# Kernel tuning notes

Measured on AMD Instinct MI355X. Metric: run time of the kernel, lower is better.

Reference implementation:

```python
import jax, jax.numpy as jnp
import numpy as np

NEG_SLOPE = 0.2
LN_EPS = 1e-6

B, L, D, H = 32, 512, 256, 4
N = B * L
E = 65536
C = D  # per-head out channels (GATConv out_channels=d_model)


def setup_inputs() -> dict:
    key = jax.random.key(0)
    ks = jax.random.split(key, 10)
    s = 1.0 / np.sqrt(D)
    inputs = jax.random.normal(ks[0], (B, L, D), dtype=jnp.float32)
    edge_index = jax.random.randint(ks[1], (2, E), 0, N, dtype=jnp.int64)
    return {
        "inputs": inputs,
        "edge_index": edge_index,
        "ln_gamma": jnp.ones((D,), jnp.float32),
        "ln_beta": jnp.zeros((D,), jnp.float32),
        "W1": jax.random.normal(ks[2], (D, D), jnp.float32) * s,   # linear_before_gnn
        "b1": jnp.zeros((D,), jnp.float32),
        "W_gat": jax.random.normal(ks[3], (H * C, D), jnp.float32) * s,  # GATConv.lin (no bias)
        "att_src": jax.random.normal(ks[4], (H, C), jnp.float32) * s,
        "att_dst": jax.random.normal(ks[5], (H, C), jnp.float32) * s,
        "bias_gat": jnp.zeros((C,), jnp.float32),  # concat=False -> size out_channels
        "W2": jax.random.normal(ks[6], (D, D), jnp.float32) * s,   # linear_after_gnn
        "b2": jnp.zeros((D,), jnp.float32),
    }


def _gat_conv(x, edge_index, W_gat, att_src, att_dst, bias_gat):
    # x: [N, D] -> project to [N, H, C]
    xh = (x @ W_gat.T).reshape(N, H, C)
    # add self loops (PyG default add_self_loops=True)
    loops = jnp.arange(N, dtype=edge_index.dtype)
    src = jnp.concatenate([edge_index[0], loops])  # message source j
    dst = jnp.concatenate([edge_index[1], loops])  # message target i
    # per-node attention logits [N, H]
    a_src = jnp.einsum("nhc,hc->nh", xh, att_src)
    a_dst = jnp.einsum("nhc,hc->nh", xh, att_dst)
    # per-edge logits and segment softmax over destination node
    e = jax.nn.leaky_relu(a_src[src] + a_dst[dst], NEG_SLOPE)  # [Etot, H]
    e_max = jax.ops.segment_max(e, dst, num_segments=N)        # every node has a self loop
    e = jnp.exp(e - e_max[dst])
    denom = jax.ops.segment_sum(e, dst, num_segments=N)
    alpha = e / denom[dst]                                     # [Etot, H]
    # weighted message aggregation (dropout on alpha skipped: eval mode)
    msg = xh[src] * alpha[:, :, None]                          # [Etot, H, C]
    out = jax.ops.segment_sum(msg, dst, num_segments=N)        # [N, H, C]
    return out.mean(axis=1) + bias_gat                         # concat=False -> head mean


def reference(inputs, edge_index, ln_gamma, ln_beta, W1, b1, W_gat, att_src, att_dst, bias_gat, W2, b2):
    # LayerNorm(eps=1e-6)
    mu = inputs.mean(-1, keepdims=True)
    var = jnp.mean((inputs - mu) ** 2, axis=-1, keepdims=True)
    x = (inputs - mu) * jax.lax.rsqrt(var + LN_EPS) * ln_gamma + ln_beta
    x = x.reshape(-1, D)
    gnn_in = x @ W1.T + b1
    gnn_out = _gat_conv(gnn_in, edge_index, W_gat, att_src, att_dst, bias_gat)
    y = gnn_out @ W2.T + b2
    # dropout is identity in eval mode; residual add
    return y.reshape(B, L, D) + inputs
```

## Files before the change

### kernel.cpp

```cpp
#include <hip/hip_runtime.h>
#include <math.h>

#define N_NODES 16384
#define D_MODEL 256
#define H_HEADS 4
#define C_CH 256
#define E_EDGES 65536
#define ETOT (E_EDGES + N_NODES)
#define HC 1024
#define MAXDEG 64
#define PSZ 262144

typedef __bf16 bf16x8 __attribute__((ext_vector_type(8)));
typedef __bf16 bf16x4 __attribute__((ext_vector_type(4)));
typedef float f32x4 __attribute__((ext_vector_type(4)));

__device__ __forceinline__ __bf16 f2bf(float f) { return (__bf16)f; }
__device__ __forceinline__ float bf2f(__bf16 b) { return (float)b; }

__global__ __launch_bounds__(256) void prep1_ln(
    const float* __restrict__ Wg, const float* __restrict__ att_src,
    const float* __restrict__ att_dst, const float* __restrict__ W2,
    const int* __restrict__ ei, const float* __restrict__ in,
    const float* __restrict__ gamma, const float* __restrict__ beta,
    float* __restrict__ t, float* __restrict__ Vp, int* __restrict__ cnt,
    int* __restrict__ csr, __bf16* __restrict__ x_ln)
{
    int b = blockIdx.x;
    int tid = threadIdx.x;
    if (b >= 1408) {
        int wave = tid >> 6, lane = tid & 63;
        int row = (b - 1408) * 4 + wave;
        float4 v = ((const float4*)(in + (size_t)row * D_MODEL))[lane];
        float s  = v.x + v.y + v.z + v.w;
        float sq = v.x*v.x + v.y*v.y + v.z*v.z + v.w*v.w;
        for (int off = 32; off; off >>= 1) {
            s  += __shfl_xor(s,  off);
            sq += __shfl_xor(sq, off);
        }
        float mean = s * (1.0f / D_MODEL);
        float var  = sq * (1.0f / D_MODEL) - mean * mean;
        float inv  = rsqrtf(var + 1e-6f);
        float4 g = ((const float4*)gamma)[lane];
        float4 bb = ((const float4*)beta)[lane];
        bf16x4 o;
        o[0] = f2bf((v.x - mean) * inv * g.x + bb.x);
        o[1] = f2bf((v.y - mean) * inv * g.y + bb.y);
        o[2] = f2bf((v.z - mean) * inv * g.z + bb.z);
        o[3] = f2bf((v.w - mean) * inv * g.w + bb.w);
        *(bf16x4*)(x_ln + (size_t)row * D_MODEL + lane * 4) = o;
        return;
    }
    if (b < 64) {
        int v = b >> 3, sl = b & 7, h = v & 3;
        const float* att = ((v < 4) ? att_src : att_dst) + h * C_CH;
        float acc = 0.f;
        #pragma unroll
        for (int j = 0; j < 32; ++j) {
            int c = sl * 32 + j;
            acc = fmaf(Wg[(size_t)(h * 256 + c) * 256 + tid], att[c], acc);
        }
        atomicAdd(&t[v * 256 + tid], acc);
        return;
    }
    if (b < 1088) {
        int bb2 = b - 64;
        int orig = bb2 >> 2, cs = bb2 & 3;
        int og = (orig & 63) * 4, h = orig >> 6;
        const float* w2r = W2 + (size_t)og * 256;
        const float* wgp = Wg + ((size_t)h * 256) * 256 + tid;
        float a0 = 0.f, a1 = 0.f, a2 = 0.f, a3 = 0.f;
        int cb = cs * 64;
        #pragma unroll 4
        for (int c = cb; c < cb + 64; ++c) {
            float wv = wgp[(size_t)c * 256];
            a0 = fmaf(w2r[c],       wv, a0);
            a1 = fmaf(w2r[256 + c], wv, a1);
            a2 = fmaf(w2r[512 + c], wv, a2);
            a3 = fmaf(w2r[768 + c], wv, a3);
        }
        size_t base = (size_t)cs * PSZ + (size_t)og * 1024 + h * 256 + tid;
        Vp[base]        = a0;
        Vp[base + 1024] = a1;
        Vp[base + 2048] = a2;
        Vp[base + 3072] = a3;
        return;
    }
    {
        int e = (b - 1088) * 256 + tid;
        int src, dst;
        if (e < E_EDGES) { src = ei[e]; dst = ei[E_EDGES + e]; }
        else             { src = dst = e - E_EDGES; }
        int pos = atomicAdd(cnt + dst, 1);
        csr[(size_t)dst * MAXDEG + pos] = src;
    }
}

__global__ __launch_bounds__(256) void prep2(
    const float* __restrict__ t, const float* __restrict__ W1,
    const float* __restrict__ b1, const float* __restrict__ Vp,
    const float* __restrict__ W2, const float* __restrict__ bg,
    const float* __restrict__ b2, float* __restrict__ u2,
    float* __restrict__ c0, float* __restrict__ Wzp,
    float* __restrict__ bias_z)
{
    __shared__ float red[4][4];
    __shared__ float vsh[4][64];
    int b = blockIdx.x;
    int d = threadIdx.x;

    if (b < 1024) {
        int orig = b >> 2, ks = b & 3;
        int og = (orig & 63) * 4, h = orig >> 6;
        int lane = d & 63, wid = d >> 6;
        int kb = ks * 64;
        size_t vbase = (size_t)og * 1024 + h * 256;

        {
            int j = d >> 6, kk = d & 63;
            float s = 0.f;
            #pragma unroll
            for (int cs = 0; cs < 4; ++cs)
                s += Vp[(size_t)cs * PSZ + vbase + (size_t)j * 1024 + kb + kk];
            vsh[j][kk] = s;
        }
        __syncthreads();

        float a0 = 0.f, a1 = 0.f, a2 = 0.f, a3 = 0.f;
        #pragma unroll 4
        for (int k = 0; k < 64; ++k) {
            float w1v = W1[(size_t)(kb + k) * 256 + d];
            a0 = fmaf(vsh[0][k], w1v, a0);
            a1 = fmaf(vsh[1][k], w1v, a1);
            a2 = fmaf(vsh[2][k], w1v, a2);
            a3 = fmaf(vsh[3][k], w1v, a3);
        }
        size_t base = (size_t)ks * PSZ + vbase + d;
        Wzp[base]        = a0;
        Wzp[base + 1024] = a1;
        Wzp[base + 2048] = a2;
        Wzp[base + 3072] = a3;

        if (ks == 0) {
            float b1v = b1[d];
            #pragma unroll
            for (int j = 0; j < 4; ++j) {
                float vsum = 0.f;
                #pragma unroll
                for (int cs = 0; cs < 4; ++cs)
                    vsum += Vp[(size_t)cs * PSZ + vbase + (size_t)j * 1024 + d];
                float p = vsum * b1v;
                for (int s = 32; s; s >>= 1) p += __shfl_xor(p, s);
                if (lane == 0) red[j][wid] = p;
            }
            __syncthreads();
            if (d < 4) {
                float s = red[d][0] + red[d][1] + red[d][2] + red[d][3];
                atomicAdd(&bias_z[og + d], 0.25f * s);
            }
            if (h == 0) {
                __syncthreads();
                float bgv = bg[d];
                #pragma unroll
                for (int j = 0; j < 4; ++j) {
                    float q = W2[(size_t)(og + j) * 256 + d] * bgv;
                    for (int s = 32; s; s >>= 1) q += __shfl_xor(q, s);
                    if (lane == 0) red[j][wid] = q;
                }
                __syncthreads();
                if (d < 4) {
                    float s = red[d][0] + red[d][1] + red[d][2] + red[d][3];
                    atomicAdd(&bias_z[og + d], s + b2[og + d]);
                }
            }
        }
        return;
    }
    {
        int bb = b - 1024;
        int v = bb >> 3, sl = bb & 7;
        const float* tv = t + v * 256;
        float acc = 0.f;
        #pragma unroll
        for (int j = 0; j < 32; ++j) {
            int k = sl * 32 + j;
            acc = fmaf(tv[k], W1[(size_t)k * 256 + d], acc);
        }
        atomicAdd(&u2[v * 256 + d], acc);
        if (d < 32) {
            float p = tv[sl * 32 + d] * b1[sl * 32 + d];
            for (int s = 16; s; s >>= 1) p += __shfl_xor(p, s);
            if (d == 0) atomicAdd(&c0[v], p);
        }
    }
}

__global__ __launch_bounds__(256) void logits_cvt(
    const __bf16* __restrict__ x_ln, const float* __restrict__ u2,
    const float* __restrict__ c0, float* __restrict__ a_src,
    float* __restrict__ a_dst, const float* __restrict__ Wzp,
    __bf16* __restrict__ Wz)
{
    int b = blockIdx.x;
    int tid = threadIdx.x;
    if (b >= 4096) {
        int idx = (b - 4096) * 256 + tid;
        float4 v = make_float4(0.f, 0.f, 0.f, 0.f);
        #pragma unroll
        for (int p = 0; p < 4; ++p) {
            float4 t4 = ((const float4*)(Wzp + (size_t)p * PSZ))[idx];
            v.x += t4.x; v.y += t4.y; v.z += t4.z; v.w += t4.w;
        }
        bf16x4 o;
        o[0] = f2bf(v.x); o[1] = f2bf(v.y); o[2] = f2bf(v.z); o[3] = f2bf(v.w);
        *(bf16x4*)(Wz + (size_t)idx * 4) = o;
        return;
    }
    __shared__ float u2s[8][256];
    __shared__ float c0s[8];
    #pragma unroll
    for (int k = 0; k < 8; ++k) u2s[k][tid] = u2[k * 256 + tid];
    if (tid < 8) c0s[tid] = c0[tid];
    __syncthreads();

    int wave = tid >> 6, lane = tid & 63;
    int n = b * 4 + wave;
    int v = lane >> 3, p = lane & 7;
    const __bf16* xp = x_ln + (size_t)n * D_MODEL + p * 32;
    const float*  up = &u2s[v][p * 32];
    float acc = 0.f;
    #pragma unroll
    for (int ti = 0; ti < 4; ++ti) {
        bf16x8 x = *(const bf16x8*)(xp + ti * 8);
        #pragma unroll
        for (int j = 0; j < 8; ++j)
            acc = fmaf(bf2f(x[j]), up[ti * 8 + j], acc);
    }
    acc += __shfl_xor(acc, 1);
    acc += __shfl_xor(acc, 2);
    acc += __shfl_xor(acc, 4);
    if (p == 0) {
        float o = acc + c0s[v];
        if (v < 4) a_src[n * H_HEADS + v] = o;
        else       a_dst[n * H_HEADS + (v - 4)] = o;
    }
}

__global__ __launch_bounds__(256) void gat_fused(
    const __bf16* __restrict__ x_ln, const float* __restrict__ a_src,
    const float* __restrict__ a_dst, const int* __restrict__ cnt,
    const int* __restrict__ csr, __bf16* __restrict__ agg)
{
    __shared__ float wsh[4][MAXDEG][4];
    int wave = threadIdx.x >> 6, lane = threadIdx.x & 63;
    int i = blockIdx.x * 4 + wave;
    int deg = cnt[i];
    int sidx = csr[(size_t)i * MAXDEG + lane];
    float4 ad = *(const float4*)(a_dst + i * H_HEADS);

    float4 wgt = make_float4(0.f, 0.f, 0.f, 0.f);
    if (lane < deg) {
        float4 as = *(const float4*)(a_src + sidx * H_HEADS);
        float l0 = as.x + ad.x, l1 = as.y + ad.y,
              l2 = as.z + ad.z, l3 = as.w + ad.w;
        l0 = (l0 > 0.f) ? l0 : 0.2f * l0;
        l1 = (l1 > 0.f) ? l1 : 0.2f * l1;
        l2 = (l2 > 0.f) ? l2 : 0.2f * l2;
        l3 = (l3 > 0.f) ? l3 : 0.2f * l3;
        wgt = make_float4(__expf(l0), __expf(l1), __expf(l2), __expf(l3));
    }
    float s0 = wgt.x, s1 = wgt.y, s2 = wgt.z, s3 = wgt.w;
    #pragma unroll
    for (int off = 32; off; off >>= 1) {
        s0 += __shfl_xor(s0, off);
        s1 += __shfl_xor(s1, off);
        s2 += __shfl_xor(s2, off);
        s3 += __shfl_xor(s3, off);
    }
    *(float4*)&wsh[wave][lane][0] = wgt;

    float acc[4][4] = {};
    for (int e0 = 0; e0 < deg; e0 += 8) {
        bf16x4 X[8];
        float4 W[8];
        #pragma unroll
        for (int j = 0; j < 8; ++j) {
            int ee = e0 + j;
            bool val = ee < deg;
            int el = val ? ee : 0;
            int s = __shfl(sidx, el);
            X[j] = *(const bf16x4*)(x_ln + (size_t)s * D_MODEL + lane * 4);
            float4 wv = *(const float4*)&wsh[wave][el][0];
            W[j] = val ? wv : make_float4(0.f, 0.f, 0.f, 0.f);
        }
        #pragma unroll
        for (int j = 0; j < 8; ++j) {
            #pragma unroll
            for (int d = 0; d < 4; ++d) {
                float xv = bf2f(X[j][d]);
                acc[0][d] = fmaf(W[j].x, xv, acc[0][d]);
                acc[1][d] = fmaf(W[j].y, xv, acc[1][d]);
                acc[2][d] = fmaf(W[j].z, xv, acc[2][d]);
                acc[3][d] = fmaf(W[j].w, xv, acc[3][d]);
            }
        }
    }
    float sc[4] = {0.25f / s0, 0.25f / s1, 0.25f / s2, 0.25f / s3};
    #pragma unroll
    for (int h = 0; h < 4; ++h) {
        bf16x4 o;
        #pragma unroll
        for (int j = 0; j < 4; ++j) o[j] = f2bf(acc[h][j] * sc[h]);
        *(bf16x4*)(agg + (size_t)i * HC + h * 256 + lane * 4) = o;
    }
}

#define APAD 72

__global__ __launch_bounds__(512) void gemm_skinny(
    const __bf16* __restrict__ A, const __bf16* __restrict__ B,
    const float* __restrict__ bias, const float* __restrict__ resid,
    float* __restrict__ outf, int K)
{
    __shared__ __align__(16) __bf16 As[64 * APAD];
    __shared__ __align__(16) __bf16 Bs[256 * APAD];
    int tid  = threadIdx.x;
    int lane = tid & 63;
    int w    = tid >> 6;
    int quad = lane >> 4;
    int l16  = lane & 15;
    int m0 = blockIdx.x * 64;
    int n0 = w * 32;

    int srow = tid >> 3, sp = tid & 7;
    const __bf16* Ab = A + (size_t)(m0 + srow) * K + sp * 8;
    const __bf16* Bb = B + (size_t)srow * K + sp * 8;
    size_t rstride = (size_t)64 * K;

    f32x4 acc[4][2] = {};

    bf16x8 a0_, b0_[4];
    bf16x8 a1_, b1_[4];

    auto compute = [&]() {
        #pragma unroll
        for (int ks = 0; ks < 2; ++ks) {
            bf16x8 af[4], bfr[2];
            #pragma unroll
            for (int mt = 0; mt < 4; ++mt)
                af[mt] = *(const bf16x8*)(As + (mt * 16 + l16) * APAD
                                          + ks * 32 + quad * 8);
            #pragma unroll
            for (int nt = 0; nt < 2; ++nt)
                bfr[nt] = *(const bf16x8*)(Bs + (n0 + nt * 16 + l16) * APAD
                                           + ks * 32 + quad * 8);
            #pragma unroll
            for (int mt = 0; mt < 4; ++mt)
                #pragma unroll
                for (int nt = 0; nt < 2; ++nt)
                    acc[mt][nt] = __builtin_amdgcn_mfma_f32_16x16x32_bf16(
                        af[mt], bfr[nt], acc[mt][nt], 0, 0, 0);
        }
    };

    a0_ = *(const bf16x8*)(Ab);
    #pragma unroll
    for (int t = 0; t < 4; ++t)
        b0_[t] = *(const bf16x8*)(Bb + t * rstride);

    for (int kb = 0; kb < K; kb += 128) {
        {
            const __bf16* Ap = Ab + kb + 64;
            const __bf16* Bp = Bb + kb + 64;
            a1_ = *(const bf16x8*)(Ap);
            #pragma unroll
            for (int t = 0; t < 4; ++t)
                b1_[t] = *(const bf16x8*)(Bp + t * rstride);
        }
        __syncthreads();
        *(bf16x8*)(As + srow * APAD + sp * 8) = a0_;
        #pragma unroll
        for (int t = 0; t < 4; ++t)
            *(bf16x8*)(Bs + (srow + t * 64) * APAD + sp * 8) = b0_[t];
        __syncthreads();
        compute();

        if (kb + 128 < K) {
            const __bf16* Ap = Ab + kb + 128;
            const __bf16* Bp = Bb + kb + 128;
            a0_ = *(const bf16x8*)(Ap);
            #pragma unroll
            for (int t = 0; t < 4; ++t)
                b0_[t] = *(const bf16x8*)(Bp + t * rstride);
        }
        __syncthreads();
        *(bf16x8*)(As + srow * APAD + sp * 8) = a1_;
        #pragma unroll
        for (int t = 0; t < 4; ++t)
            *(bf16x8*)(Bs + (srow + t * 64) * APAD + sp * 8) = b1_[t];
        __syncthreads();
        compute();
    }

    #pragma unroll
    for (int nt = 0; nt < 2; ++nt) {
        int col = n0 + nt * 16 + l16;
        float bv = bias[col];
        #pragma unroll
        for (int mt = 0; mt < 4; ++mt) {
            int row = m0 + mt * 16 + quad * 4;
            #pragma unroll
            for (int r = 0; r < 4; ++r) {
                size_t off = (size_t)(row + r) * C_CH + col;
                outf[off] = acc[mt][nt][r] + bv + resid[off];
            }
        }
    }
}

extern "C" void kernel_launch(void* const* d_in, const int* in_sizes, int n_in,
                              void* d_out, int out_size, void* d_ws, size_t ws_size,
                              hipStream_t stream)
{
    const float* inp      = (const float*)d_in[0];
    const int*   ei       = (const int*)  d_in[1];
    const float* ln_gamma = (const float*)d_in[2];
    const float* ln_beta  = (const float*)d_in[3];
    const float* W1       = (const float*)d_in[4];
    const float* b1       = (const float*)d_in[5];
    const float* W_gat    = (const float*)d_in[6];
    const float* att_src  = (const float*)d_in[7];
    const float* att_dst  = (const float*)d_in[8];
    const float* bias_gat = (const float*)d_in[9];
    const float* W2       = (const float*)d_in[10];
    const float* b2       = (const float*)d_in[11];

    char* ws = (char*)d_ws;
    __bf16* x_ln_bf = (__bf16*)(ws);
    __bf16* agg_bf  = (__bf16*)(ws + (8ull  << 20));
    __bf16* Wz_b    = (__bf16*)(ws + (40ull << 20));
    float*  a_src_b = (float*)(ws + (41ull << 20));
    float*  a_dst_b = a_src_b + (size_t)N_NODES * H_HEADS;
    float*  t_vec   = (float*)(ws + (42ull << 20));
    float*  u2      = t_vec + 2048;
    float*  c0      = u2 + 2048;
    float*  bias_z  = c0 + 8;
    int*    cnt     = (int*)(bias_z + 256);
    int*    csr     = (int*)(ws + (45ull << 20));
    float*  Vp      = (float*)(ws + (49ull << 20));
    float*  Wzp     = (float*)(ws + (57ull << 20));

    size_t zbytes = (2048 + 2048 + 8 + 256) * sizeof(float)
                  + N_NODES * sizeof(int);
    hipMemsetAsync(t_vec, 0, zbytes, stream);

    prep1_ln<<<1408 + 4096, 256, 0, stream>>>(W_gat, att_src, att_dst, W2, ei,
                                              inp, ln_gamma, ln_beta,
                                              t_vec, Vp, cnt, csr, x_ln_bf);
    prep2<<<1088, 256, 0, stream>>>(t_vec, W1, b1, Vp, W2, bias_gat, b2,
                                    u2, c0, Wzp, bias_z);
    logits_cvt<<<4096 + 256, 256, 0, stream>>>(x_ln_bf, u2, c0,
                                               a_src_b, a_dst_b, Wzp, Wz_b);
    gat_fused<<<N_NODES / 4, 256, 0, stream>>>(x_ln_bf, a_src_b, a_dst_b,
                                               cnt, csr, agg_bf);
    gemm_skinny<<<N_NODES / 64, 512, 0, stream>>>(agg_bf, Wz_b, bias_z, inp,
                                                  (float*)d_out, HC);
}
```

Measured before the change: 155.6 us.

## Fuse GAT aggregation into the output GEMM via shared-memory tile

Merges the per-node attention aggregation kernel with the skinny output GEMM. Each 512-thread block aggregates 64 nodes into a padded bf16 LDS tile, then runs MFMA against Wz read directly from global memory, so the 32MB agg buffer is never written to or read back from HBM. Attention weights now move between lanes by shuffles instead of through LDS. The cost is less parallelism: 256 blocks of 512 threads with a ~132KB LDS tile, likely one block per CU, and the GEMM phase has no global-load pipelining of Wz.

```diff
diff --git a/kernel.cpp b/kernel.cpp
--- a/kernel.cpp
+++ b/kernel.cpp
@@ -246,173 +246,122 @@
     }
 }
 
-__global__ __launch_bounds__(256) void gat_fused(
+#define TPAD 1032
+
+__global__ __launch_bounds__(512, 1) void gat_gemm(
     const __bf16* __restrict__ x_ln, const float* __restrict__ a_src,
     const float* __restrict__ a_dst, const int* __restrict__ cnt,
-    const int* __restrict__ csr, __bf16* __restrict__ agg)
+    const int* __restrict__ csr, const __bf16* __restrict__ Wz,
+    const float* __restrict__ bias_z, const float* __restrict__ resid,
+    float* __restrict__ outf)
 {
-    __shared__ float wsh[4][MAXDEG][4];
-    int wave = threadIdx.x >> 6, lane = threadIdx.x & 63;
-    int i = blockIdx.x * 4 + wave;
-    int deg = cnt[i];
-    int sidx = csr[(size_t)i * MAXDEG + lane];
-    float4 ad = *(const float4*)(a_dst + i * H_HEADS);
-
-    float4 wgt = make_float4(0.f, 0.f, 0.f, 0.f);
-    if (lane < deg) {
-        float4 as = *(const float4*)(a_src + sidx * H_HEADS);
-        float l0 = as.x + ad.x, l1 = as.y + ad.y,
-              l2 = as.z + ad.z, l3 = as.w + ad.w;
-        l0 = (l0 > 0.f) ? l0 : 0.2f * l0;
-        l1 = (l1 > 0.f) ? l1 : 0.2f * l1;
-        l2 = (l2 > 0.f) ? l2 : 0.2f * l2;
-        l3 = (l3 > 0.f) ? l3 : 0.2f * l3;
-        wgt = make_float4(__expf(l0), __expf(l1), __expf(l2), __expf(l3));
-    }
-    float s0 = wgt.x, s1 = wgt.y, s2 = wgt.z, s3 = wgt.w;
-    #pragma unroll
-    for (int off = 32; off; off >>= 1) {
-        s0 += __shfl_xor(s0, off);
-        s1 += __shfl_xor(s1, off);
-        s2 += __shfl_xor(s2, off);
-        s3 += __shfl_xor(s3, off);
-    }
-    *(float4*)&wsh[wave][lane][0] = wgt;
-
-    float acc[4][4] = {};
-    for (int e0 = 0; e0 < deg; e0 += 8) {
-        bf16x4 X[8];
-        float4 W[8];
-        #pragma unroll
-        for (int j = 0; j < 8; ++j) {
-            int ee = e0 + j;
-            bool val = ee < deg;
-            int el = val ? ee : 0;
-            int s = __shfl(sidx, el);
-            X[j] = *(const bf16x4*)(x_ln + (size_t)s * D_MODEL + lane * 4);
-            float4 wv = *(const float4*)&wsh[wave][el][0];
-            W[j] = val ? wv : make_float4(0.f, 0.f, 0.f, 0.f);
-        }
-        #pragma unroll
-        for (int j = 0; j < 8; ++j) {
-            #pragma unroll
-            for (int d = 0; d < 4; ++d) {
-                float xv = bf2f(X[j][d]);
-                acc[0][d] = fmaf(W[j].x, xv, acc[0][d]);
-                acc[1][d] = fmaf(W[j].y, xv, acc[1][d]);
-                acc[2][d] = fmaf(W[j].z, xv, acc[2][d]);
-                acc[3][d] = fmaf(W[j].w, xv, acc[3][d]);
-            }
-        }
-    }
-    float sc[4] = {0.25f / s0, 0.25f / s1, 0.25f / s2, 0.25f / s3};
-    #pragma unroll
-    for (int h = 0; h < 4; ++h) {
-        bf16x4 o;
-        #pragma unroll
-        for (int j = 0; j < 4; ++j) o[j] = f2bf(acc[h][j] * sc[h]);
-        *(bf16x4*)(agg + (size_t)i * HC + h * 256 + lane * 4) = o;
-    }
-}
-
-#define APAD 72
-
-__global__ __launch_bounds__(512) void gemm_skinny(
-    const __bf16* __restrict__ A, const __bf16* __restrict__ B,
-    const float* __restrict__ bias, const float* __restrict__ resid,
-    float* __restrict__ outf, int K)
-{
-    __shared__ __align__(16) __bf16 As[64 * APAD];
-    __shared__ __align__(16) __bf16 Bs[256 * APAD];
-    int tid  = threadIdx.x;
-    int lane = tid & 63;
-    int w    = tid >> 6;
-    int quad = lane >> 4;
-    int l16  = lane & 15;
+    __shared__ __align__(16) __bf16 T[64 * TPAD];
+    int tid = threadIdx.x;
+    int lane = tid & 63, w = tid >> 6;
     int m0 = blockIdx.x * 64;
+
+    #pragma unroll 2
+    for (int nn = 0; nn < 8; ++nn) {
+        int node = w * 8 + nn;
+        int i = m0 + node;
+        int deg = cnt[i];
+        int sidx = csr[(size_t)i * MAXDEG + lane];
+        float4 ad = *(const float4*)(a_dst + i * H_HEADS);
+
+        float4 wgt = make_float4(0.f, 0.f, 0.f, 0.f);
+        if (lane < deg) {
+            float4 as = *(const float4*)(a_src + sidx * H_HEADS);
+            float l0 = as.x + ad.x, l1 = as.y + ad.y,
+                  l2 = as.z + ad.z, l3 = as.w + ad.w;
+            l0 = (l0 > 0.f) ? l0 : 0.2f * l0;
+            l1 = (l1 > 0.f) ? l1 : 0.2f * l1;
+            l2 = (l2 > 0.f) ? l2 : 0.2f * l2;
+            l3 = (l3 > 0.f) ? l3 : 0.2f * l3;
+            wgt = make_float4(__expf(l0), __expf(l1), __expf(l2), __expf(l3));
+        }
+        float s0 = wgt.x, s1 = wgt.y, s2 = wgt.z, s3 = wgt.w;
+        #pragma unroll
+        for (int off = 32; off; off >>= 1) {
+            s0 += __shfl_xor(s0, off);
+            s1 += __shfl_xor(s1, off);
+            s2 += __shfl_xor(s2, off);
+            s3 += __shfl_xor(s3, off);
+        }
+
+        float acc[4][4] = {};
+        for (int e0 = 0; e0 < deg; e0 += 8) {
+            bf16x4 X[8];
+            float4 W[8];
+            #pragma unroll
+            for (int j = 0; j < 8; ++j) {
+                int ee = e0 + j;
+                bool val = ee < deg;
+                int el = val ? ee : 0;
+                int s = __shfl(sidx, el);
+                X[j] = *(const bf16x4*)(x_ln + (size_t)s * D_MODEL + lane * 4);
+                float4 wv;
+                wv.x = __shfl(wgt.x, el);
+                wv.y = __shfl(wgt.y, el);
+                wv.z = __shfl(wgt.z, el);
+                wv.w = __shfl(wgt.w, el);
+                W[j] = val ? wv : make_float4(0.f, 0.f, 0.f, 0.f);
+            }
+            #pragma unroll
+            for (int j = 0; j < 8; ++j) {
+                #pragma unroll
+                for (int d = 0; d < 4; ++d) {
+                    float xv = bf2f(X[j][d]);
+                    acc[0][d] = fmaf(W[j].x, xv, acc[0][d]);
+                    acc[1][d] = fmaf(W[j].y, xv, acc[1][d]);
+                    acc[2][d] = fmaf(W[j].z, xv, acc[2][d]);
+                    acc[3][d] = fmaf(W[j].w, xv, acc[3][d]);
+                }
+            }
+        }
+        float sc[4] = {0.25f / s0, 0.25f / s1, 0.25f / s2, 0.25f / s3};
+        #pragma unroll
+        for (int h = 0; h < 4; ++h) {
+            bf16x4 o;
+            #pragma unroll
+            for (int j = 0; j < 4; ++j) o[j] = f2bf(acc[h][j] * sc[h]);
+            *(bf16x4*)(T + node * TPAD + h * 256 + lane * 4) = o;
+        }
+    }
+    __syncthreads();
+
+    int quad = lane >> 4, l16 = lane & 15;
     int n0 = w * 32;
-
-    int srow = tid >> 3, sp = tid & 7;
-    const __bf16* Ab = A + (size_t)(m0 + srow) * K + sp * 8;
-    const __bf16* Bb = B + (size_t)srow * K + sp * 8;
-    size_t rstride = (size_t)64 * K;
-
-    f32x4 acc[4][2] = {};
-
-    bf16x8 a0_, b0_[4];
-    bf16x8 a1_, b1_[4];
-
-    auto compute = [&]() {
-        #pragma unroll
-        for (int ks = 0; ks < 2; ++ks) {
-            bf16x8 af[4], bfr[2];
-            #pragma unroll
-            for (int mt = 0; mt < 4; ++mt)
-                af[mt] = *(const bf16x8*)(As + (mt * 16 + l16) * APAD
-                                          + ks * 32 + quad * 8);
+    f32x4 pacc[4][2] = {};
+    #pragma unroll 4
+    for (int kk = 0; kk < HC; kk += 32) {
+        bf16x8 af[4], bfr[2];
+        #pragma unroll
+        for (int mt = 0; mt < 4; ++mt)
+            af[mt] = *(const bf16x8*)(T + (mt * 16 + l16) * TPAD
+                                      + kk + quad * 8);
+        #pragma unroll
+        for (int nt = 0; nt < 2; ++nt)
+            bfr[nt] = *(const bf16x8*)(Wz + (size_t)(n0 + nt * 16 + l16) * HC
+                                       + kk + quad * 8);
+        #pragma unroll
+        for (int mt = 0; mt < 4; ++mt)
             #pragma unroll
             for (int nt = 0; nt < 2; ++nt)
-                bfr[nt] = *(const bf16x8*)(Bs + (n0 + nt * 16 + l16) * APAD
-                                           + ks * 32 + quad * 8);
-            #pragma unroll
-            for (int mt = 0; mt < 4; ++mt)
-                #pragma unroll
-                for (int nt = 0; nt < 2; ++nt)
-                    acc[mt][nt] = __builtin_amdgcn_mfma_f32_16x16x32_bf16(
-                        af[mt], bfr[nt], acc[mt][nt], 0, 0, 0);
-        }
-    };
-
-    a0_ = *(const bf16x8*)(Ab);
-    #pragma unroll
-    for (int t = 0; t < 4; ++t)
-        b0_[t] = *(const bf16x8*)(Bb + t * rstride);
-
-    for (int kb = 0; kb < K; kb += 128) {
-        {
-            const __bf16* Ap = Ab + kb + 64;
-            const __bf16* Bp = Bb + kb + 64;
-            a1_ = *(const bf16x8*)(Ap);
-            #pragma unroll
-            for (int t = 0; t < 4; ++t)
-                b1_[t] = *(const bf16x8*)(Bp + t * rstride);
-        }
-        __syncthreads();
-        *(bf16x8*)(As + srow * APAD + sp * 8) = a0_;
-        #pragma unroll
-        for (int t = 0; t < 4; ++t)
-            *(bf16x8*)(Bs + (srow + t * 64) * APAD + sp * 8) = b0_[t];
-        __syncthreads();
-        compute();
-
-        if (kb + 128 < K) {
-            const __bf16* Ap = Ab + kb + 128;
-            const __bf16* Bp = Bb + kb + 128;
-            a0_ = *(const bf16x8*)(Ap);
-            #pragma unroll
-            for (int t = 0; t < 4; ++t)
-                b0_[t] = *(const bf16x8*)(Bp + t * rstride);
-        }
-        __syncthreads();
-        *(bf16x8*)(As + srow * APAD + sp * 8) = a1_;
-        #pragma unroll
-        for (int t = 0; t < 4; ++t)
-            *(bf16x8*)(Bs + (srow + t * 64) * APAD + sp * 8) = b1_[t];
-        __syncthreads();
-        compute();
+                pacc[mt][nt] = __builtin_amdgcn_mfma_f32_16x16x32_bf16(
+                    af[mt], bfr[nt], pacc[mt][nt], 0, 0, 0);
     }
 
     #pragma unroll
     for (int nt = 0; nt < 2; ++nt) {
         int col = n0 + nt * 16 + l16;
-        float bv = bias[col];
+        float bv = bias_z[col];
         #pragma unroll
         for (int mt = 0; mt < 4; ++mt) {
             int row = m0 + mt * 16 + quad * 4;
             #pragma unroll
             for (int r = 0; r < 4; ++r) {
                 size_t off = (size_t)(row + r) * C_CH + col;
-                outf[off] = acc[mt][nt][r] + bv + resid[off];
+                outf[off] = pacc[mt][nt][r] + bv + resid[off];
             }
         }
     }
@@ -437,7 +386,6 @@
 
     char* ws = (char*)d_ws;
     __bf16* x_ln_bf = (__bf16*)(ws);
-    __bf16* agg_bf  = (__bf16*)(ws + (8ull  << 20));
     __bf16* Wz_b    = (__bf16*)(ws + (40ull << 20));
     float*  a_src_b = (float*)(ws + (41ull << 20));
     float*  a_dst_b = a_src_b + (size_t)N_NODES * H_HEADS;
@@ -461,8 +409,7 @@
                                     u2, c0, Wzp, bias_z);
     logits_cvt<<<4096 + 256, 256, 0, stream>>>(x_ln_bf, u2, c0,
                                                a_src_b, a_dst_b, Wzp, Wz_b);
-    gat_fused<<<N_NODES / 4, 256, 0, stream>>>(x_ln_bf, a_src_b, a_dst_b,
-                                               cnt, csr, agg_bf);
-    gemm_skinny<<<N_NODES / 64, 512, 0, stream>>>(agg_bf, Wz_b, bias_z, inp,
-                                                  (float*)d_out, HC);
+    gat_gemm<<<N_NODES / 64, 512, 0, stream>>>(x_ln_bf, a_src_b, a_dst_b,
+                                               cnt, csr, Wz_b, bias_z,
+                                               inp, (float*)d_out);
 }
```

Result: no change. 154.5 us (-0.7%).
